# Kernel optimization log

Hardware: AMD Instinct MI355X
Metric: run time of the kernel (lower is better)

The kernel has to match this reference:

```python
import jax, jax.numpy as jnp
import numpy as np
from jax import lax

B, C, H, Wd = 8, 3, 256, 256
K = 32           # kernels
LAT = K * 8      # 256, latent dim
P = 7            # patch size
HALF = P // 2
S = 1024         # samples per image
PD = C * P * P   # 147
NEG = 0.01       # LeakyReLU slope
EPS = 1e-5


def setup_inputs() -> dict:
    key = jax.random.key(0)
    ks = jax.random.split(key, 20)
    x = jax.random.normal(ks[0], (B, C, H, Wd), dtype=jnp.float32)
    # patch centers must satisfy HALF <= c <= H-1-HALF (here [3, 252])
    anchors_hw = jax.random.randint(ks[1], (B, S, 2), HALF, H - HALF, dtype=jnp.int32)
    positives_hw = jax.random.randint(ks[2], (B, S, 2), HALF, H - HALF, dtype=jnp.int32)
    def w(k, shape, fan_in):
        return jax.random.normal(k, shape, dtype=jnp.float32) * (1.0 / np.sqrt(fan_in))
    inp = dict(x=x, anchors_hw=anchors_hw, positives_hw=positives_hw,
               w1=w(ks[3], (K, C, 3, 3), C * 9),        g1=jnp.ones((K,), jnp.float32),        b1=jnp.zeros((K,), jnp.float32),
               w2=w(ks[4], (2 * K, K, 3, 3), K * 9),    g2=jnp.ones((2 * K,), jnp.float32),    b2=jnp.zeros((2 * K,), jnp.float32),
               w3=w(ks[5], (4 * K, 2 * K, 3, 3), 2 * K * 9), g3=jnp.ones((4 * K,), jnp.float32), b3=jnp.zeros((4 * K,), jnp.float32),
               w4=w(ks[6], (8 * K, 4 * K, 3, 3), 4 * K * 9), g4=jnp.ones((8 * K,), jnp.float32), b4=jnp.zeros((8 * K,), jnp.float32),
               lin1_w=w(ks[7], (PD, LAT), LAT), lin1_b=jnp.zeros((PD,), jnp.float32),
               lin2_w=w(ks[8], (PD, PD), PD),   lin2_b=jnp.zeros((PD,), jnp.float32))
    return inp


def _conv(x, w):
    return lax.conv_general_dilated(x, w, (1, 1), 'SAME',
                                    dimension_numbers=('NCHW', 'OIHW', 'NCHW'))


def _bn(x, g, b):
    # training-mode BatchNorm2d: batch stats over (N,H,W)
    m = x.mean(axis=(0, 2, 3), keepdims=True)
    v = x.var(axis=(0, 2, 3), keepdims=True)
    return g[None, :, None, None] * (x - m) * lax.rsqrt(v + EPS) + b[None, :, None, None]


def _lrelu(x):
    return jnp.where(x >= 0, x, NEG * x)


def _forward(x, anchors_hw, positives_hw, w1, g1, b1, w2, g2, b2, w3, g3, b3,
             w4, g4, b4, lin1_w, lin1_b, lin2_w, lin2_b):
    feat = _lrelu(_bn(_conv(x, w1), g1, b1))
    feat = _lrelu(_bn(_conv(feat, w2), g2, b2))
    feat = _lrelu(_bn(_conv(feat, w3), g3, b3))
    feat = _lrelu(_bn(_conv(feat, w4), g4, b4))  # [B, LAT, H, W]

    fhwc = jnp.transpose(feat, (0, 2, 3, 1))  # [B,H,W,LAT]
    gather_pts = jax.vmap(lambda f, hw: f[hw[:, 0], hw[:, 1]])  # per-batch fancy gather
    W_anchors = gather_pts(fhwc, anchors_hw)      # [B,S,LAT]
    W_positives = gather_pts(fhwc, positives_hw)  # [B,S,LAT]

    def slice_one(img, hw):  # img [C,H,W], hw [2]
        return lax.dynamic_slice(img, (0, hw[0] - HALF, hw[1] - HALF), (C, P, P))
    patch_real = jax.vmap(jax.vmap(slice_one, in_axes=(None, 0)))(x, anchors_hw)  # [B,S,C,P,P]

    h = _lrelu(jnp.einsum('bsl,pl->bsp', W_anchors, lin1_w) + lin1_b)
    patch_recon = (jnp.einsum('bsp,qp->bsq', h, lin2_w) + lin2_b).reshape(x.shape[0], -1, C, P, P)
    return (feat, patch_real, patch_recon, W_anchors, W_positives)


def reference(x, anchors_hw, positives_hw, w1, g1, b1, w2, g2, b2, w3, g3, b3,
              w4, g4, b4, lin1_w, lin1_b, lin2_w, lin2_b):
    return _forward(x, anchors_hw, positives_hw, w1, g1, b1, w2, g2, b2,
                    w3, g3, b3, w4, g4, b4, lin1_w, lin1_b, lin2_w, lin2_b)
```

## Files before the change

kernel.cpp:

```cpp
#include <hip/hip_runtime.h>
#include <hip/hip_bf16.h>

typedef unsigned short u16;
typedef short bf16x8 __attribute__((ext_vector_type(8)));
typedef float f32x4 __attribute__((ext_vector_type(4)));
typedef unsigned short u16x8 __attribute__((ext_vector_type(8)));

#define PD 147

static const long OFF_PREAL = 134217728L;
static const long OFF_PRECON= 135421952L;
static const long OFF_WA    = 136626176L;
static const long OFF_WP    = 138723328L;

static const long RAW_SPLIT = 100663296L;

__device__ __forceinline__ float lrelu(float v){ return v >= 0.f ? v : 0.01f*v; }

__device__ __forceinline__ float bf2f(u16 u){
    union { unsigned int i; float f; } x; x.i = ((unsigned int)u) << 16; return x.f;
}
__device__ __forceinline__ u16 f2bf(float f){
    __hip_bfloat16 h = __float2bfloat16(f);
    return *reinterpret_cast<u16*>(&h);
}

__device__ __forceinline__ void gload16(const void* g, void* l){
    __builtin_amdgcn_global_load_lds((const __attribute__((address_space(1))) void*)g,
                                     (__attribute__((address_space(3))) void*)l, 16, 0, 0);
}

template<int CIN, int KOUT, bool SPLIT>
__global__ __launch_bounds__(256, 4)
void conv_mfma(const u16* __restrict__ fin, const u16* __restrict__ wt,
               const float* __restrict__ ssin,
               void* __restrict__ out_, u16* __restrict__ rawhi,
               float* __restrict__ part)
{
    constexpr int CC = CIN / 32;
    constexpr int NSTEPS = CC * 9;
    constexpr int ABYTES = 324 * 32 * 2;
    constexpr int BBYTES = 2 * 64 * 32 * 2;
    constexpr int EPIB = 256 * 64 * 2;
    constexpr int SB = (ABYTES + BBYTES) > EPIB ? (ABYTES + BBYTES) : EPIB;
    __shared__ __align__(16) char smem[SB];
    u16* As = (u16*)smem;
    u16* Bs = (u16*)(smem + ABYTES);

    const int tid = threadIdx.x;
    const int w = tid >> 6, lane = tid & 63;
    const int tile = blockIdx.x;
    const int tx0 = (tile & 15) << 4, ty0 = (tile >> 4) << 4;
    const int bz = blockIdx.y;
    const int b  = blockIdx.z;
    const long pixbase = (long)b << 16;
    const int hi = lane >> 4;
    const int quarter = tid & 3;

    f32x4 acc[4][4];
#pragma unroll
    for (int m = 0; m < 4; m++)
#pragma unroll
        for (int n = 0; n < 4; n++) acc[m][n] = (f32x4){0.f,0.f,0.f,0.f};

    auto stage_a = [&](int cc){
        float sc8[8], sh8[8];
        int c0 = cc*32 + quarter*8;
#pragma unroll
        for (int j = 0; j < 8; j++){
            sc8[j] = ssin[c0 + j];
            sh8[j] = ssin[CIN + c0 + j];
        }
#pragma unroll
        for (int r = 0; r < 6; ++r){
            int q = r*256 + tid;
            if (q < 1296){
                int pf = q >> 2;
                int ly = pf / 18, lx = pf - ly*18;
                int gy = ty0 + ly - 1, gx = tx0 + lx - 1;
                u16x8 o = (u16x8){0,0,0,0,0,0,0,0};
                if ((unsigned)gy < 256u && (unsigned)gx < 256u){
                    u16x8 v = *(const u16x8*)(fin + ((pixbase + (gy<<8) + gx) * CIN + cc*32 + quarter*8));
#pragma unroll
                    for (int j = 0; j < 8; j++)
                        o[j] = f2bf(lrelu(sc8[j]*bf2f(v[j]) + sh8[j]));
                }
                *(u16x8*)(As + q*8) = o;
            }
        }
    };
    auto stage_b = [&](int s, int buf){
        int cc2 = s / 9, tap = s - cc2*9;
        const u16* src = wt + (((long)tap*KOUT + bz*64 + (tid>>2)) * CIN + cc2*32 + (tid&3)*8);
        u16* dst = Bs + buf*2048 + (w*64)*8;
        gload16(src, dst);
    };

    stage_a(0);
    stage_b(0, 0);
    __syncthreads();

#pragma unroll 1
    for (int s = 0; s < NSTEPS; ++s){
        int cc = s / 9, tap = s - cc*9;
        if (s + 1 < NSTEPS) stage_b(s + 1, (s + 1) & 1);

        int dy = tap / 3, dx = tap - dy*3;
        const u16* Bb = Bs + (s & 1) * 2048;
        bf16x8 av[4];
#pragma unroll
        for (int m = 0; m < 4; m++){
            int pf = (w*4 + m + dy)*18 + (lane & 15) + dx;
            av[m] = *(const bf16x8*)(As + pf*32 + hi*8);
        }
        bf16x8 bv[4];
#pragma unroll
        for (int n = 0; n < 4; n++){
            int chl = n*16 + (lane & 15);
            bv[n] = *(const bf16x8*)(Bb + chl*32 + hi*8);
        }
#pragma unroll
        for (int m = 0; m < 4; m++)
#pragma unroll
            for (int n = 0; n < 4; n++)
                acc[m][n] = __builtin_amdgcn_mfma_f32_16x16x32_bf16(av[m], bv[n], acc[m][n], 0, 0, 0);

        __syncthreads();
        if (tap == 8 && cc + 1 < CC){
            stage_a(cc + 1);
            __syncthreads();
        }
    }

    {
        float* sred = (float*)smem;
#pragma unroll
        for (int n = 0; n < 4; n++){
            float s = 0.f, s2 = 0.f;
#pragma unroll
            for (int m = 0; m < 4; m++)
#pragma unroll
                for (int j = 0; j < 4; j++){
                    float v = acc[m][n][j];
                    s += v; s2 += v*v;
                }
            s += __shfl_down(s, 32); s2 += __shfl_down(s2, 32);
            s += __shfl_down(s, 16); s2 += __shfl_down(s2, 16);
            if (lane < 16){
                int ch = n*16 + lane;
                sred[w*64 + ch]       = s;
                sred[256 + w*64 + ch] = s2;
            }
        }
        __syncthreads();
        if (tid < 64){
            float S = 0.f, S2 = 0.f;
#pragma unroll
            for (int w2 = 0; w2 < 4; w2++){
                S  += sred[w2*64 + tid];
                S2 += sred[256 + w2*64 + tid];
            }
            long i = (long)b*256 + tile;
            long off = (i*KOUT + bz*64 + tid)*2;
            part[off]   = S;
            part[off+1] = S2;
        }
        __syncthreads();
    }

    {
        u16* ep = (u16*)smem;
#pragma unroll
        for (int m = 0; m < 4; m++)
#pragma unroll
            for (int n = 0; n < 4; n++){
                int ch = n*16 + (lane & 15);
#pragma unroll
                for (int j = 0; j < 4; j++){
                    int px = (w*4 + m)*16 + (lane>>4)*4 + j;
                    ep[px*64 + ch] = f2bf(acc[m][n][j]);
                }
            }
        __syncthreads();
        u16* outh = (u16*)out_;
        if (SPLIT && b >= 6) outh = rawhi - RAW_SPLIT;
#pragma unroll
        for (int it = 0; it < 8; ++it){
            int i = it*256 + tid;
            int px = i >> 3, u = i & 7;
            int py = px >> 4, pxc = px & 15;
            long ga = (pixbase + ((ty0+py)<<8) + tx0 + pxc) * KOUT + bz*64 + (long)u*8;
            *(int4*)(outh + ga) = *(int4*)(ep + (long)i*8);
        }
    }
}

__global__ __launch_bounds__(256)
void conv1_direct(const float* __restrict__ x, const float* __restrict__ w1, u16* __restrict__ f1)
{
    __shared__ float wl[864];
    const int t = threadIdx.x;
    for (int i = t; i < 864; i += 256) wl[i] = w1[i];
    __syncthreads();
    const int y = blockIdx.x, b = blockIdx.y;
    float acc[32];
#pragma unroll
    for (int k = 0; k < 32; k++) acc[k] = 0.f;
    const long ib = (long)b*3*65536;
    for (int c = 0; c < 3; c++){
#pragma unroll
        for (int dy = 0; dy < 3; dy++){
            int gy = y + dy - 1;
#pragma unroll
            for (int dx = 0; dx < 3; dx++){
                int gx = t + dx - 1;
                float v = 0.f;
                if ((unsigned)gy < 256u && (unsigned)gx < 256u)
                    v = x[ib + c*65536 + (gy<<8) + gx];
                const float* wp = &wl[c*9 + dy*3 + dx];
#pragma unroll
                for (int k = 0; k < 32; k++) acc[k] += v * wp[k*27];
            }
        }
    }
    u16 ub[32];
#pragma unroll
    for (int k = 0; k < 32; k++) ub[k] = f2bf(acc[k]);
    u16* dst = f1 + ((long)(b*65536 + (y<<8) + t)) * 32;
#pragma unroll
    for (int j = 0; j < 4; j++) *(int4*)(dst + j*8) = *(int4*)(ub + j*8);
}

__global__ __launch_bounds__(256)
void prep_w(const float* __restrict__ w, u16* __restrict__ wt, int K, int C)
{
    int i = blockIdx.x*256 + threadIdx.x;
    if (i >= 9*K*C) return;
    int c = i % C; int r = i / C; int k = r % K; int tap = r / K;
    wt[i] = f2bf(w[((long)k*C + c)*9 + tap]);
}

template<int C>
__global__ __launch_bounds__(256)
void bn_stats_nhwc(const u16* __restrict__ f, float* __restrict__ part)
{
    constexpr int CQ = C/4;
    constexpr int SUBS = 256/CQ;
    const int t = threadIdx.x;
    const int cq = t & (CQ-1);
    const int sub = t / CQ;
    const long rowbase = (long)blockIdx.x * 512;
    float s[4] = {0,0,0,0}, q2[4] = {0,0,0,0};
    for (int r = sub; r < 512; r += SUBS){
        ushort4 v = *(const ushort4*)(f + (rowbase + r)*C + cq*4);
        float x0 = bf2f(v.x), x1 = bf2f(v.y), x2 = bf2f(v.z), x3 = bf2f(v.w);
        s[0]+=x0; q2[0]+=x0*x0; s[1]+=x1; q2[1]+=x1*x1;
        s[2]+=x2; q2[2]+=x2*x2; s[3]+=x3; q2[3]+=x3*x3;
    }
    __shared__ float r0[256], r1[256];
    for (int j = 0; j < 4; j++){
        r0[t] = s[j]; r1[t] = q2[j];
        __syncthreads();
        for (int st = 128; st >= CQ; st >>= 1){
            if (t < st){ r0[t] += r0[t+st]; r1[t] += r1[t+st]; }
            __syncthreads();
        }
        if (t < CQ){
            part[((long)blockIdx.x * C + t*4 + j)*2]     = r0[t];
            part[((long)blockIdx.x * C + t*4 + j)*2 + 1] = r1[t];
        }
        __syncthreads();
    }
}

__global__ __launch_bounds__(256)
void bn_stats_final2(const float* __restrict__ part, const float* __restrict__ g,
                     const float* __restrict__ bb, int C, int NB2, float* __restrict__ ss)
{
    const int c = blockIdx.x, t = threadIdx.x;
    float s = 0.f, s2 = 0.f;
    for (int i = t; i < NB2; i += 256){
        s  += part[((long)i*C + c)*2];
        s2 += part[((long)i*C + c)*2 + 1];
    }
    __shared__ float r0[256], r1[256];
    r0[t] = s; r1[t] = s2;
    __syncthreads();
    for (int st = 128; st > 0; st >>= 1){
        if (t < st){ r0[t] += r0[t+st]; r1[t] += r1[t+st]; }
        __syncthreads();
    }
    if (t == 0){
        const float invN = 1.f/524288.f;
        float m = r0[0]*invN;
        float v = r1[0]*invN - m*m;
        float sc = g[c]/sqrtf(v + 1e-5f);
        ss[c] = sc; ss[C+c] = bb[c] - m*sc;
    }
}

__global__ __launch_bounds__(256)
void bn_expand_t(const u16* __restrict__ rawlo, const u16* __restrict__ rawhi,
                 const float* __restrict__ ss, float* __restrict__ feat, int b0)
{
    __shared__ u16 lds[64*258];
    const int bid = blockIdx.x;
    const int b = b0 + (bid >> 10);
    const int px0 = (bid & 1023) * 64;
    const long p0 = (((long)(b<<16) + px0)) << 8;
    const u16* src = (b < 6) ? (rawlo + p0) : (rawhi + (p0 - RAW_SPLIT));
    const int t = threadIdx.x;
#pragma unroll
    for (int it = 0; it < 8; ++it){
        int i = it*256 + t;
        int px = i >> 5, u = i & 31;
        *(u16x8*)&lds[px*258 + u*8] = *(const u16x8*)(src + (long)i*8);
    }
    __syncthreads();
#pragma unroll
    for (int it = 0; it < 16; ++it){
        int idx = it*256 + t;
        int ch = idx >> 4;
        int q  = idx & 15;
        const float sc = ss[ch], sh = ss[256 + ch];
        float4 o;
        o.x = lrelu(sc*bf2f(lds[(q*4+0)*258 + ch]) + sh);
        o.y = lrelu(sc*bf2f(lds[(q*4+1)*258 + ch]) + sh);
        o.z = lrelu(sc*bf2f(lds[(q*4+2)*258 + ch]) + sh);
        o.w = lrelu(sc*bf2f(lds[(q*4+3)*258 + ch]) + sh);
        *(float4*)(feat + (((long)(b*256 + ch)) << 16) + px0 + q*4) = o;
    }
}

__global__ __launch_bounds__(256)
void gather_w_raw(const u16* __restrict__ rawlo, const u16* __restrict__ rawhi,
                  const float* __restrict__ ss, const int* __restrict__ hw,
                  float* __restrict__ outW)
{
    const int site = blockIdx.x;
    const int b = site >> 10;
    const int y = hw[site*2], x = hw[site*2 + 1];
    const int c = threadIdx.x;
    const long p = ((long)((b<<16) + (y<<8) + x)) << 8;
    const u16* base = (b < 6) ? (rawlo + p) : (rawhi + (p - RAW_SPLIT));
    float v = bf2f(base[c]);
    outW[(long)site*256 + c] = lrelu(ss[c]*v + ss[256 + c]);
}

__global__ __launch_bounds__(256)
void gather_patch(const float* __restrict__ x, const int* __restrict__ hw,
                  float* __restrict__ out)
{
    const long i = (long)blockIdx.x*256 + threadIdx.x;
    if (i >= 1204224L) return;
    const int px = (int)(i % 7);
    long r = i / 7;
    const int py = (int)(r % 7); r /= 7;
    const int c  = (int)(r % 3); r /= 3;
    const int s  = (int)(r % 1024);
    const int b  = (int)(r / 1024);
    const int site = b*1024 + s;
    const int yy = hw[site*2]     - 3 + py;
    const int xx = hw[site*2 + 1] - 3 + px;
    out[i] = x[(((long)(b*3 + c)) << 16) + ((long)yy << 8) + xx];
}

__global__ __launch_bounds__(256)
void mlp8(const float* __restrict__ Wa, const float* __restrict__ l1w,
          const float* __restrict__ l1b, const float* __restrict__ l2w,
          const float* __restrict__ l2b, float* __restrict__ out)
{
    __shared__ float wa[2048];
    __shared__ float h[8][152];
    const int blk = blockIdx.x;
    const int t = threadIdx.x;
#pragma unroll
    for (int it = 0; it < 8; ++it)
        wa[it*256 + t] = Wa[(long)blk*2048 + it*256 + t];
    __syncthreads();
    if (t < PD){
        float a[8] = {0,0,0,0,0,0,0,0};
        const float* wr = l1w + t*256;
#pragma unroll 4
        for (int l = 0; l < 256; ++l){
            float wv = wr[l];
#pragma unroll
            for (int g = 0; g < 8; ++g) a[g] += wa[g*256 + l]*wv;
        }
        float bb = l1b[t];
#pragma unroll
        for (int g = 0; g < 8; ++g) h[g][t] = lrelu(a[g] + bb);
    }
    __syncthreads();
    if (t < PD){
        float r[8] = {0,0,0,0,0,0,0,0};
        const float* wr = l2w + t*PD;
        for (int p = 0; p < PD; ++p){
            float wv = wr[p];
#pragma unroll
            for (int g = 0; g < 8; ++g) r[g] += h[g][p]*wv;
        }
        float bb = l2b[t];
#pragma unroll
        for (int g = 0; g < 8; ++g)
            out[((long)(blk*8 + g))*PD + t] = r[g] + bb;
    }
}

extern "C" void kernel_launch(void* const* d_in, const int* in_sizes, int n_in,
                              void* d_out, int out_size, void* d_ws, size_t ws_size,
                              hipStream_t stream)
{
    const float* x   = (const float*)d_in[0];
    const int*   anc = (const int*)  d_in[1];
    const int*   pos = (const int*)  d_in[2];
    const float* w1  = (const float*)d_in[3];
    const float* g1  = (const float*)d_in[4];
    const float* b1  = (const float*)d_in[5];
    const float* w2  = (const float*)d_in[6];
    const float* g2  = (const float*)d_in[7];
    const float* b2  = (const float*)d_in[8];
    const float* w3  = (const float*)d_in[9];
    const float* g3  = (const float*)d_in[10];
    const float* b3  = (const float*)d_in[11];
    const float* w4  = (const float*)d_in[12];
    const float* g4  = (const float*)d_in[13];
    const float* b4  = (const float*)d_in[14];
    const float* l1w = (const float*)d_in[15];
    const float* l1b = (const float*)d_in[16];
    const float* l2w = (const float*)d_in[17];
    const float* l2b = (const float*)d_in[18];

    float* feat = (float*)d_out;
    float* oPR  = feat + OFF_PREAL;
    float* oRC  = feat + OFF_PRECON;
    float* oWA  = feat + OFF_WA;
    float* oWP  = feat + OFF_WP;

    char* wsb = (char*)d_ws;
    u16* f2b = (u16*)wsb;
    u16* f3b = (u16*)(wsb + 67108864L);
    u16* f1b = (u16*)(wsb + 134217728L);

    u16* rawlo = (u16*)d_out + 167772160L;
    u16* rawhi = f2b;

    u16* Wt2 = (u16*)oWA;
    u16* Wt3 = Wt2 + 18432;
    u16* Wt4 = Wt3 + 73728;
    float* part = oWP;
    float* ss1 = oRC, *ss2 = oRC + 64, *ss3 = oRC + 192, *ss4 = oRC + 448;

    prep_w<<<72,   256, 0, stream>>>(w2, Wt2, 64, 32);
    prep_w<<<288,  256, 0, stream>>>(w3, Wt3, 128, 64);
    prep_w<<<1152, 256, 0, stream>>>(w4, Wt4, 256, 128);

    conv1_direct<<<dim3(256,8), 256, 0, stream>>>(x, w1, f1b);
    bn_stats_nhwc<32><<<1024, 256, 0, stream>>>(f1b, part);
    bn_stats_final2<<<32, 256, 0, stream>>>(part, g1, b1, 32, 1024, ss1);

    conv_mfma<32,64,false><<<dim3(256,1,8), 256, 0, stream>>>(f1b, Wt2, ss1, f2b, nullptr, part);
    bn_stats_final2<<<64, 256, 0, stream>>>(part, g2, b2, 64, 2048, ss2);

    conv_mfma<64,128,false><<<dim3(256,2,8), 256, 0, stream>>>(f2b, Wt3, ss2, f3b, nullptr, part);
    bn_stats_final2<<<128, 256, 0, stream>>>(part, g3, b3, 128, 2048, ss3);

    conv_mfma<128,256,true><<<dim3(256,4,8), 256, 0, stream>>>(f3b, Wt4, ss3, rawlo, rawhi, part);
    bn_stats_final2<<<256, 256, 0, stream>>>(part, g4, b4, 256, 2048, ss4);

    gather_w_raw<<<8192, 256, 0, stream>>>(rawlo, rawhi, ss4, anc, oWA);
    gather_w_raw<<<8192, 256, 0, stream>>>(rawlo, rawhi, ss4, pos, oWP);
    gather_patch<<<4704, 256, 0, stream>>>(x, anc, oPR);

    bn_expand_t<<<5120, 256, 0, stream>>>(rawlo, rawhi, ss4, feat, 0);
    bn_expand_t<<<1024, 256, 0, stream>>>(rawlo, rawhi, ss4, feat, 5);
    bn_expand_t<<<2048, 256, 0, stream>>>(rawlo, rawhi, ss4, feat, 6);

    mlp8<<<1024, 256, 0, stream>>>(oWA, l1w, l1b, l2w, l2b, oRC);
}
```

Baseline: 766.5 us.

## Load conv weights directly into registers instead of LDS double buffer

```diff
diff --git a/kernel.cpp b/kernel.cpp
--- a/kernel.cpp
+++ b/kernel.cpp
@@ -25,27 +25,19 @@
     return *reinterpret_cast<u16*>(&h);
 }
 
-__device__ __forceinline__ void gload16(const void* g, void* l){
-    __builtin_amdgcn_global_load_lds((const __attribute__((address_space(1))) void*)g,
-                                     (__attribute__((address_space(3))) void*)l, 16, 0, 0);
-}
-
 template<int CIN, int KOUT, bool SPLIT>
-__global__ __launch_bounds__(256, 4)
+__global__ __launch_bounds__(256, 3)
 void conv_mfma(const u16* __restrict__ fin, const u16* __restrict__ wt,
                const float* __restrict__ ssin,
                void* __restrict__ out_, u16* __restrict__ rawhi,
                float* __restrict__ part)
 {
     constexpr int CC = CIN / 32;
-    constexpr int NSTEPS = CC * 9;
     constexpr int ABYTES = 324 * 32 * 2;
-    constexpr int BBYTES = 2 * 64 * 32 * 2;
     constexpr int EPIB = 256 * 64 * 2;
-    constexpr int SB = (ABYTES + BBYTES) > EPIB ? (ABYTES + BBYTES) : EPIB;
+    constexpr int SB = ABYTES > EPIB ? ABYTES : EPIB;
     __shared__ __align__(16) char smem[SB];
     u16* As = (u16*)smem;
-    u16* Bs = (u16*)(smem + ABYTES);
 
     const int tid = threadIdx.x;
     const int w = tid >> 6, lane = tid & 63;
@@ -89,48 +81,45 @@
             }
         }
     };
-    auto stage_b = [&](int s, int buf){
-        int cc2 = s / 9, tap = s - cc2*9;
-        const u16* src = wt + (((long)tap*KOUT + bz*64 + (tid>>2)) * CIN + cc2*32 + (tid&3)*8);
-        u16* dst = Bs + buf*2048 + (w*64)*8;
-        gload16(src, dst);
+
+    auto load_b = [&](int cc2, int tap, bf16x8* dst){
+#pragma unroll
+        for (int n = 0; n < 4; n++){
+            int ch = bz*64 + n*16 + (lane & 15);
+            dst[n] = *(const bf16x8*)(wt + (((long)tap*KOUT + ch) * CIN + cc2*32 + hi*8));
+        }
     };
 
     stage_a(0);
-    stage_b(0, 0);
     __syncthreads();
 
 #pragma unroll 1
-    for (int s = 0; s < NSTEPS; ++s){
-        int cc = s / 9, tap = s - cc*9;
-        if (s + 1 < NSTEPS) stage_b(s + 1, (s + 1) & 1);
-
-        int dy = tap / 3, dx = tap - dy*3;
-        const u16* Bb = Bs + (s & 1) * 2048;
-        bf16x8 av[4];
-#pragma unroll
-        for (int m = 0; m < 4; m++){
-            int pf = (w*4 + m + dy)*18 + (lane & 15) + dx;
-            av[m] = *(const bf16x8*)(As + pf*32 + hi*8);
-        }
-        bf16x8 bv[4];
-#pragma unroll
-        for (int n = 0; n < 4; n++){
-            int chl = n*16 + (lane & 15);
-            bv[n] = *(const bf16x8*)(Bb + chl*32 + hi*8);
-        }
-#pragma unroll
-        for (int m = 0; m < 4; m++)
-#pragma unroll
-            for (int n = 0; n < 4; n++)
-                acc[m][n] = __builtin_amdgcn_mfma_f32_16x16x32_bf16(av[m], bv[n], acc[m][n], 0, 0, 0);
-
-        __syncthreads();
-        if (tap == 8 && cc + 1 < CC){
+    for (int cc = 0; cc < CC; ++cc){
+        bf16x8 bvreg[2][4];
+        load_b(cc, 0, bvreg[0]);
+#pragma unroll
+        for (int tap = 0; tap < 9; ++tap){
+            if (tap + 1 < 9) load_b(cc, tap + 1, bvreg[(tap + 1) & 1]);
+            const int dy = tap / 3, dx = tap - dy*3;
+            bf16x8 av[4];
+#pragma unroll
+            for (int m = 0; m < 4; m++){
+                int pf = (w*4 + m + dy)*18 + (lane & 15) + dx;
+                av[m] = *(const bf16x8*)(As + pf*32 + hi*8);
+            }
+#pragma unroll
+            for (int m = 0; m < 4; m++)
+#pragma unroll
+                for (int n = 0; n < 4; n++)
+                    acc[m][n] = __builtin_amdgcn_mfma_f32_16x16x32_bf16(av[m], bvreg[tap & 1][n], acc[m][n], 0, 0, 0);
+        }
+        if (cc + 1 < CC){
+            __syncthreads();
             stage_a(cc + 1);
             __syncthreads();
         }
     }
+    __syncthreads();
 
     {
         float* sred = (float*)smem;
```

Result: slower. 1.269 ms (+65.6%).
